# Performance work log

Measured on AMD Instinct MI355X. Metric: run time of the kernel, lower is better.

## Reference

```python
import jax, jax.numpy as jnp
import numpy as np

V, S, D, H = 32000, 1024, 768, 3072
EPS = 1e-5


def pos_encoding(seq_len, dim, dtype=jnp.float32):
    # pe[pos, i] = sin(pos/10000^(i/dim)) if i even else cos(pos/10000^(i/dim))
    pos = jnp.arange(seq_len, dtype=dtype)[:, None]
    i = jnp.arange(dim, dtype=dtype)[None, :]
    ang = pos / jnp.power(jnp.asarray(10000.0, dtype), i / dim)
    even = (jnp.arange(dim) % 2 == 0)[None, :]
    return jnp.where(even, jnp.sin(ang), jnp.cos(ang))


def layernorm2d(x, w, b):
    # normalizes over last two dims (token_size, input_dim), affine params [S, D]
    m = jnp.mean(x, axis=(-2, -1), keepdims=True)
    v = jnp.mean((x - m) ** 2, axis=(-2, -1), keepdims=True)
    return (x - m) / jnp.sqrt(v + EPS) * w + b


def setup_inputs() -> dict:
    key = jax.random.key(0)
    ks = jax.random.split(key, 16)
    sc = 0.02
    emb = jax.random.normal(ks[0], (V, D), jnp.float32) * sc
    emb = emb.at[0].set(0.0)  # padding_idx=0
    inp = {
        "x": jax.random.randint(ks[1], (8, S), 0, V),
        "emb": emb,
        "Wq": jax.random.normal(ks[2], (D, H), jnp.float32) * sc,
        "bq": jnp.zeros((H,), jnp.float32),
        "Wk": jax.random.normal(ks[3], (D, H), jnp.float32) * sc,
        "bk": jnp.zeros((H,), jnp.float32),
        "Wv": jax.random.normal(ks[4], (D, H), jnp.float32) * sc,
        "bv": jnp.zeros((H,), jnp.float32),
        "Wo": jax.random.normal(ks[5], (H, D), jnp.float32) * sc,
        "bo": jnp.zeros((D,), jnp.float32),
        "W1": jax.random.normal(ks[6], (D, H), jnp.float32) * sc,
        "b1": jnp.zeros((H,), jnp.float32),
        "W2": jax.random.normal(ks[7], (H, D), jnp.float32) * sc,
        "b2": jnp.zeros((D,), jnp.float32),
        "ln1_w": jnp.ones((S, D), jnp.float32),
        "ln1_b": jnp.zeros((S, D), jnp.float32),
        "ln2_w": jnp.ones((S, D), jnp.float32),
        "ln2_b": jnp.zeros((S, D), jnp.float32),
    }
    return inp


def reference(x, emb, Wq, bq, Wk, bk, Wv, bv, Wo, bo, W1, b1, W2, b2, ln1_w, ln1_b, ln2_w, ln2_b):
    y = emb[x]                                   # [B, S, D]
    y = y + pos_encoding(y.shape[1], y.shape[2], y.dtype)
    # unscaled self-attention (no 1/sqrt(d) factor, faithful to source)
    q = y @ Wq + bq
    k = y @ Wk + bk
    v = y @ Wv + bv
    attn = jax.nn.softmax(jnp.einsum("bsh,bth->bst", q, k), axis=-1)
    a = jnp.einsum("bst,bth->bsh", attn, v) @ Wo + bo
    y = layernorm2d(y + a, ln1_w, ln1_b)
    # FFN: GELU applied AFTER second linear (faithful to source)
    f = jax.nn.gelu((y @ W1 + b1) @ W2 + b2, approximate=False)
    y = layernorm2d(y + f, ln2_w, ln2_b)
    return y
```

## Files before the change

### kernel.cpp

```cpp
#include <hip/hip_runtime.h>
#include <hip/hip_fp16.h>

#define DI __device__ __forceinline__

typedef _Float16 f16x8 __attribute__((ext_vector_type(8)));
typedef float f32x4 __attribute__((ext_vector_type(4)));

struct alignas(8) h4 { __half x, y, z, w; };

DI void async16(const void* g, void* l) {
  __builtin_amdgcn_global_load_lds(
      (__attribute__((address_space(1))) void*)g,
      (__attribute__((address_space(3))) void*)l, 16, 0, 0);
}

DI float waveReduceSum(float v) {
#pragma unroll
  for (int i = 1; i < 64; i <<= 1) v += __shfl_xor(v, i);
  return v;
}
DI float waveReduceMax(float v) {
#pragma unroll
  for (int i = 1; i < 64; i <<= 1) v = fmaxf(v, __shfl_xor(v, i));
  return v;
}

DI float gelu_exact(float x) { return 0.5f * x * (1.f + erff(x * 0.70710678118654752f)); }

template <typename CT, bool BIAS, bool BROW>
__global__ __launch_bounds__(512, 2) void gemm_nt8(
    const __half* __restrict__ A, int lda, long long sA,
    const __half* __restrict__ Bt, int ldb, long long sB,
    const float* __restrict__ bias, long long sBias,
    CT* __restrict__ C, int ldc, long long sC,
    int nT, int K) {
  __shared__ __align__(16) __half As[2][16384];
  __shared__ __align__(16) __half Bs[2][16384];

  const int tid = threadIdx.x;
  const int wave = tid >> 6, lane = tid & 63;

  const int gsz = 4 * nT;
  const int g = blockIdx.x / gsz, r = blockIdx.x % gsz;
  const int m0 = (g * 4 + (r & 3)) * 256;
  const int n0 = (r >> 2) * 256;

  A += (long long)blockIdx.z * sA;
  Bt += (long long)blockIdx.z * sB;
  C += (long long)blockIdx.z * sC;
  if constexpr (BIAS || BROW) bias += (long long)blockIdx.z * sBias;

  const int wm = wave >> 2, wn = wave & 3;

  f32x4 acc[8][4];
#pragma unroll
  for (int i = 0; i < 8; ++i)
#pragma unroll
    for (int j = 0; j < 4; ++j) acc[i][j] = (f32x4){0.f, 0.f, 0.f, 0.f};

  const int srow = tid >> 3;
  const int gc = (tid & 7) ^ (srow & 7);
  const __half* Ag = A + (size_t)(m0 + srow) * lda + gc * 8;
  const __half* Bg = Bt + (size_t)(n0 + srow) * ldb + gc * 8;
  const size_t a64 = (size_t)64 * lda, b64 = (size_t)64 * ldb;
  char* AsWr = (char*)As + wave * 1024 + lane * 16;
  char* BsWr = (char*)Bs + wave * 1024 + lane * 16;

  f16x8 sra[4], srb[4];

#define LDG(t)                                                        \
  {                                                                   \
    const __half* sa_ = Ag + (t) * 64;                                \
    const __half* sb_ = Bg + (t) * 64;                                \
    sra[0] = *(const f16x8*)(sa_);                                    \
    sra[1] = *(const f16x8*)(sa_ + a64);                              \
    sra[2] = *(const f16x8*)(sa_ + 2 * a64);                          \
    sra[3] = *(const f16x8*)(sa_ + 3 * a64);                          \
    srb[0] = *(const f16x8*)(sb_);                                    \
    srb[1] = *(const f16x8*)(sb_ + b64);                              \
    srb[2] = *(const f16x8*)(sb_ + 2 * b64);                          \
    srb[3] = *(const f16x8*)(sb_ + 3 * b64);                          \
  }
#define DSW(t)                                                        \
  {                                                                   \
    char* da_ = AsWr + (((t) & 1) ? 32768 : 0);                       \
    char* db_ = BsWr + (((t) & 1) ? 32768 : 0);                       \
    *(f16x8*)(da_) = sra[0];                                          \
    *(f16x8*)(da_ + 8192) = sra[1];                                   \
    *(f16x8*)(da_ + 16384) = sra[2];                                  \
    *(f16x8*)(da_ + 24576) = sra[3];                                  \
    *(f16x8*)(db_) = srb[0];                                          \
    *(f16x8*)(db_ + 8192) = srb[1];                                   \
    *(f16x8*)(db_ + 16384) = srb[2];                                  \
    *(f16x8*)(db_ + 24576) = srb[3];                                  \
  }

  const int ml = lane & 15, q = lane >> 4, lx = lane & 7;
  const int co0 = (q ^ lx) * 16, co1 = co0 ^ 64;
  const char* Ar = (const char*)As + wm * 16384 + ml * 128;
  const char* Br = (const char*)Bs + (wn >> 1) * 16384 + (wn & 1) * 8192 + ml * 128;

  const int nt = K >> 6;
  LDG(0);
  DSW(0);
  if (nt > 1) LDG(1);
  asm volatile("s_waitcnt lgkmcnt(0)" ::: "memory");
  __builtin_amdgcn_s_barrier();
  __builtin_amdgcn_sched_barrier(0);

  for (int t = 0; t < nt; ++t) {
    if (t + 1 < nt) {
      DSW(t + 1);
      if (t + 2 < nt) LDG(t + 2);
    }
    const int pb = (t & 1) ? 32768 : 0;
    const char* Ap = Ar + pb;
    const char* Bp = Br + pb;
    f16x8 af[8], bf[4];
#pragma unroll
    for (int ks = 0; ks < 2; ++ks) {
      const int co = ks ? co1 : co0;
#pragma unroll
      for (int i = 0; i < 8; ++i) af[i] = *(const f16x8*)(Ap + i * 2048 + co);
#pragma unroll
      for (int j = 0; j < 4; ++j) bf[j] = *(const f16x8*)(Bp + j * 2048 + co);
#pragma unroll
      for (int i = 0; i < 8; ++i)
#pragma unroll
        for (int j = 0; j < 4; ++j)
          acc[i][j] = __builtin_amdgcn_mfma_f32_16x16x32_f16(bf[j], af[i], acc[i][j], 0, 0, 0);
    }
    asm volatile("s_waitcnt lgkmcnt(0)" ::: "memory");
    __builtin_amdgcn_s_barrier();
    __builtin_amdgcn_sched_barrier(0);
  }
#undef LDG
#undef DSW

#pragma unroll
  for (int j = 0; j < 4; ++j) {
    const int col0 = n0 + wn * 64 + j * 16 + q * 4;
    float4 bc = {0.f, 0.f, 0.f, 0.f};
    if constexpr (BIAS) bc = *(const float4*)(bias + col0);
#pragma unroll
    for (int i = 0; i < 8; ++i) {
      const int row = m0 + wm * 128 + i * 16 + ml;
      const float br = BROW ? bias[row] : 0.f;
      const float v0 = acc[i][j][0] + bc.x + br;
      const float v1 = acc[i][j][1] + bc.y + br;
      const float v2 = acc[i][j][2] + bc.z + br;
      const float v3 = acc[i][j][3] + bc.w + br;
      if constexpr (sizeof(CT) == 4) {
        *(float4*)(C + (size_t)row * ldc + col0) = make_float4(v0, v1, v2, v3);
      } else {
        h4 o{__float2half(v0), __float2half(v1), __float2half(v2), __float2half(v3)};
        *(h4*)((__half*)C + (size_t)row * ldc + col0) = o;
      }
    }
  }
}

template <typename CT, bool BIAS, bool BROW>
__global__ __launch_bounds__(256) void gemm_nt(
    const __half* __restrict__ A, int lda, long long sA,
    const __half* __restrict__ Bt, int ldb, long long sB,
    const float* __restrict__ bias, long long sBias,
    CT* __restrict__ C, int ldc, long long sC,
    int nT, int K) {
  __shared__ __align__(16) __half As[128 * 64];
  __shared__ __align__(16) __half Bs[128 * 64];

  const int tid = threadIdx.x;
  const int wave = tid >> 6, lane = tid & 63;

  const int gsz = 8 * nT;
  const int g = blockIdx.x / gsz, r = blockIdx.x % gsz;
  const int m0 = (g * 8 + (r & 7)) * 128;
  const int n0 = (r >> 3) * 128;

  A += (long long)blockIdx.z * sA;
  Bt += (long long)blockIdx.z * sB;
  C += (long long)blockIdx.z * sC;
  if constexpr (BIAS || BROW) bias += (long long)blockIdx.z * sBias;
  const int wm = wave & 1, wn = wave >> 1;

  f32x4 acc[4][4];
#pragma unroll
  for (int i = 0; i < 4; ++i)
#pragma unroll
    for (int jj = 0; jj < 4; ++jj) acc[i][jj] = (f32x4){0.f, 0.f, 0.f, 0.f};

  const int srow = tid >> 3;
  const int gc = (tid & 7) ^ (srow & 7);
  const __half* Ag = A + (size_t)(m0 + srow) * lda + gc * 8;
  const __half* Bg = Bt + (size_t)(n0 + srow) * ldb + gc * 8;
  const size_t a32 = (size_t)32 * lda, b32 = (size_t)32 * ldb;
  char* AsW = (char*)As + wave * 1024;
  char* BsW = (char*)Bs + wave * 1024;

  const int ml = lane & 15, q = lane >> 4, lx = lane & 7;
  const int aoff = ((wm * 64 + ml) * 8 + (q ^ lx)) * 16;
  const int boff = ((wn * 64 + ml) * 8 + (q ^ lx)) * 16;

  for (int k0 = 0; k0 < K; k0 += 64) {
#pragma unroll
    for (int i = 0; i < 4; ++i) {
      async16(Ag + i * a32 + k0, AsW + i * 4096);
      async16(Bg + i * b32 + k0, BsW + i * 4096);
    }
    __syncthreads();
#pragma unroll
    for (int jj = 0; jj < 2; ++jj) {
      const char* Ab = (const char*)As + (jj ? (aoff ^ 64) : aoff);
      const char* Bb = (const char*)Bs + (jj ? (boff ^ 64) : boff);
      f16x8 af[4], bf[4];
#pragma unroll
      for (int i = 0; i < 4; ++i) {
        af[i] = *(const f16x8*)(Ab + i * 2048);
        bf[i] = *(const f16x8*)(Bb + i * 2048);
      }
#pragma unroll
      for (int i = 0; i < 4; ++i)
#pragma unroll
        for (int jn = 0; jn < 4; ++jn)
          acc[i][jn] = __builtin_amdgcn_mfma_f32_16x16x32_f16(bf[jn], af[i], acc[i][jn], 0, 0, 0);
    }
    __syncthreads();
  }

#pragma unroll
  for (int jn = 0; jn < 4; ++jn) {
    const int col0 = n0 + wn * 64 + jn * 16 + q * 4;
    float4 bc = {0.f, 0.f, 0.f, 0.f};
    if constexpr (BIAS) bc = *(const float4*)(bias + col0);
#pragma unroll
    for (int i = 0; i < 4; ++i) {
      const int row = m0 + wm * 64 + i * 16 + ml;
      const float br = BROW ? bias[row] : 0.f;
      const float v0 = acc[i][jn][0] + bc.x + br;
      const float v1 = acc[i][jn][1] + bc.y + br;
      const float v2 = acc[i][jn][2] + bc.z + br;
      const float v3 = acc[i][jn][3] + bc.w + br;
      if constexpr (sizeof(CT) == 4) {
        *(float4*)(C + (size_t)row * ldc + col0) = make_float4(v0, v1, v2, v3);
      } else {
        h4 o{__float2half(v0), __float2half(v1), __float2half(v2), __float2half(v3)};
        *(h4*)((__half*)C + (size_t)row * ldc + col0) = o;
      }
    }
  }
}

__global__ __launch_bounds__(256) void prep(
    const float* __restrict__ Wq, const float* __restrict__ Wk,
    const float* __restrict__ Wv, const float* __restrict__ W1,
    const float* __restrict__ Wo, const float* __restrict__ W2,
    const float* __restrict__ bq, const float* __restrict__ bk,
    __half* __restrict__ wD, __half* __restrict__ wB, __half* __restrict__ wC,
    __half* __restrict__ wA, float* __restrict__ bqk) {
  if (blockIdx.x == 2304) {
    if (blockIdx.y == 0)
      for (int i = threadIdx.x; i < 3072; i += 256) {
        bqk[i] = bq[i];
        bqk[3072 + i] = bk[i];
      }
    return;
  }
  __shared__ float t[32][33];
  const int tx = threadIdx.x & 31, ty = threadIdx.x >> 5;
  if (blockIdx.y < 4) {
    const float* in;
    __half* out;
    switch (blockIdx.y) {
      case 0: in = Wq; out = wD; break;
      case 1: in = Wk; out = wD + 3072 * 768; break;
      case 2: in = Wv; out = wB; break;
      default: in = W1; out = wC; break;
    }
    const int cb = blockIdx.x % 96, rb = blockIdx.x / 96;
    const int c = cb * 32 + tx, r0 = rb * 32;
#pragma unroll
    for (int i = 0; i < 32; i += 8) t[ty + i][tx] = in[(size_t)(r0 + ty + i) * 3072 + c];
    __syncthreads();
    const int oc = r0 + tx, o0 = cb * 32;
#pragma unroll
    for (int i = 0; i < 32; i += 8)
      out[(size_t)(o0 + ty + i) * 768 + oc] = __float2half(t[tx][ty + i]);
  } else {
    const float* in = (blockIdx.y == 5) ? W2 : Wo;
    __half* out = wA + ((blockIdx.y == 5) ? 3072 * 768 : 0);
    const int cb = blockIdx.x % 24, rb = blockIdx.x / 24;
    const int c = cb * 32 + tx, r0 = rb * 32;
#pragma unroll
    for (int i = 0; i < 32; i += 8) t[ty + i][tx] = in[(size_t)(r0 + ty + i) * 768 + c];
    __syncthreads();
    const int oc = r0 + tx, o0 = cb * 32;
#pragma unroll
    for (int i = 0; i < 32; i += 8)
      out[(size_t)(o0 + ty + i) * 3072 + oc] = __float2half(t[tx][ty + i]);
  }
}

__global__ __launch_bounds__(256) void embed_pos_kernel(
    const int* __restrict__ x, const float* __restrict__ emb,
    float* __restrict__ y, __half* __restrict__ yh) {
  const int row = blockIdx.x;
  const int s = row & 1023;
  const int tok = x[row];
  const float* ep = emb + (size_t)tok * 768;
  float* yp = y + (size_t)row * 768;
  __half* hp = yh + (size_t)row * 768;
  const float c = -13.287712379549449f / 768.f;
  for (int d = threadIdx.x; d < 768; d += 256) {
    float ang = (float)s * exp2f((float)d * c);
    float pe = (d & 1) ? cosf(ang) : sinf(ang);
    float v = ep[d] + pe;
    yp[d] = v;
    hp[d] = __float2half(v);
  }
}

__global__ __launch_bounds__(256) void softmax_rows(
    const float* __restrict__ L, __half* __restrict__ P) {
  const size_t row = blockIdx.x;
  const float4 x = ((const float4*)(L + row * 1024))[threadIdx.x];
  const int wave = threadIdx.x >> 6, lane = threadIdx.x & 63;
  float m = fmaxf(fmaxf(x.x, x.y), fmaxf(x.z, x.w));
  m = waveReduceMax(m);
  __shared__ float sm[4];
  __shared__ float ssum[4];
  if (lane == 0) sm[wave] = m;
  __syncthreads();
  m = fmaxf(fmaxf(sm[0], sm[1]), fmaxf(sm[2], sm[3]));
  float e0 = expf(x.x - m), e1 = expf(x.y - m), e2 = expf(x.z - m), e3 = expf(x.w - m);
  float s = e0 + e1 + e2 + e3;
  s = waveReduceSum(s);
  if (lane == 0) ssum[wave] = s;
  __syncthreads();
  s = ssum[0] + ssum[1] + ssum[2] + ssum[3];
  const float inv = 1.f / s;
  h4 o{__float2half(e0 * inv), __float2half(e1 * inv), __float2half(e2 * inv),
       __float2half(e3 * inv)};
  ((h4*)(P + row * 1024))[threadIdx.x] = o;
}

template <bool GELU>
__global__ __launch_bounds__(256) void residual_stats(
    float* __restrict__ y, const float* __restrict__ p0, const float* __restrict__ p1,
    const float* __restrict__ bias, float2* __restrict__ partials) {
  const int b = blockIdx.y, chunk = blockIdx.x;
  const size_t base = (size_t)b * 786432 + (size_t)chunk * 8192;
  float4* yp = (float4*)(y + base);
  const float4* a0 = (const float4*)(p0 + base);
  const float4* a1 = (const float4*)(p1 + base);
  float s = 0.f, ss = 0.f;
#pragma unroll
  for (int it = 0; it < 8; ++it) {
    const int idx = it * 256 + threadIdx.x;
    const int d = (chunk * 8192 + it * 1024 + threadIdx.x * 4) % 768;
    float4 yv = yp[idx];
    float4 v0 = a0[idx];
    float4 v1 = a1[idx];
    const float4 bv = *(const float4*)(bias + d);
    float ax = v0.x + v1.x + bv.x, ay = v0.y + v1.y + bv.y;
    float az = v0.z + v1.z + bv.z, aw = v0.w + v1.w + bv.w;
    if constexpr (GELU) {
      ax = gelu_exact(ax); ay = gelu_exact(ay);
      az = gelu_exact(az); aw = gelu_exact(aw);
    }
    float4 r{yv.x + ax, yv.y + ay, yv.z + az, yv.w + aw};
    yp[idx] = r;
    s += r.x + r.y + r.z + r.w;
    ss += r.x * r.x + r.y * r.y + r.z * r.z + r.w * r.w;
  }
  s = waveReduceSum(s);
  ss = waveReduceSum(ss);
  __shared__ float2 wr[4];
  const int wave = threadIdx.x >> 6, lane = threadIdx.x & 63;
  if (lane == 0) wr[wave] = make_float2(s, ss);
  __syncthreads();
  if (threadIdx.x == 0) {
    float S = wr[0].x + wr[1].x + wr[2].x + wr[3].x;
    float SS = wr[0].y + wr[1].y + wr[2].y + wr[3].y;
    partials[b * 96 + chunk] = make_float2(S, SS);
  }
}

template <bool WB>
__global__ __launch_bounds__(256) void ln_apply(
    float* __restrict__ y, __half* __restrict__ yh, const float* __restrict__ w,
    const float* __restrict__ bb, const float2* __restrict__ partials) {
  const unsigned i4 = blockIdx.x * 256 + threadIdx.x;
  const unsigned i = i4 * 4;
  const unsigned b = i / 786432u;
  const int tid = threadIdx.x;
  float s = 0.f, ss = 0.f;
  if (tid < 96) {
    float2 p = partials[b * 96 + tid];
    s = p.x;
    ss = p.y;
  }
  s = waveReduceSum(s);
  ss = waveReduceSum(ss);
  __shared__ float2 wsum[4];
  if ((tid & 63) == 0) wsum[tid >> 6] = make_float2(s, ss);
  __syncthreads();
  const float S = wsum[0].x + wsum[1].x + wsum[2].x + wsum[3].x;
  const float SS = wsum[0].y + wsum[1].y + wsum[2].y + wsum[3].y;
  const float inv = 1.f / 786432.f;
  const float mean = S * inv;
  const float rstd = rsqrtf(SS * inv - mean * mean + 1e-5f);

  const unsigned e4 = (i - b * 786432u) >> 2;
  float4 yv = ((const float4*)y)[i4];
  const float4 wv = ((const float4*)w)[e4];
  const float4 bv = ((const float4*)bb)[e4];
  float4 r;
  r.x = (yv.x - mean) * rstd * wv.x + bv.x;
  r.y = (yv.y - mean) * rstd * wv.y + bv.y;
  r.z = (yv.z - mean) * rstd * wv.z + bv.z;
  r.w = (yv.w - mean) * rstd * wv.w + bv.w;
  ((float4*)y)[i4] = r;
  if constexpr (WB) {
    h4 o{__float2half(r.x), __float2half(r.y), __float2half(r.z), __float2half(r.w)};
    ((h4*)yh)[i4] = o;
  }
}

extern "C" void kernel_launch(void* const* d_in, const int* in_sizes, int n_in,
                              void* d_out, int out_size, void* d_ws, size_t ws_size,
                              hipStream_t stream) {
  const int* x = (const int*)d_in[0];
  const float* emb = (const float*)d_in[1];
  const float* Wq = (const float*)d_in[2];
  const float* bq = (const float*)d_in[3];
  const float* Wk = (const float*)d_in[4];
  const float* bk = (const float*)d_in[5];
  const float* Wv = (const float*)d_in[6];
  const float* bv = (const float*)d_in[7];
  const float* Wo = (const float*)d_in[8];
  const float* bo = (const float*)d_in[9];
  const float* W1 = (const float*)d_in[10];
  const float* b1 = (const float*)d_in[11];
  const float* W2 = (const float*)d_in[12];
  const float* b2 = (const float*)d_in[13];
  const float* ln1w = (const float*)d_in[14];
  const float* ln1b = (const float*)d_in[15];
  const float* ln2w = (const float*)d_in[16];
  const float* ln2b = (const float*)d_in[17];

  float* y = (float*)d_out;

  char* ws = (char*)d_ws;
  __half* yh = (__half*)(ws + 0);
  __half* qb = (__half*)(ws + 12582912);
  __half* kb = (__half*)(ws + 62914560);
  __half* Ph = kb;
  __half* vT = (__half*)(ws + 113246208);
  float* abuf = (float*)vT;
  float* Lg = (float*)(ws + 163577856);
  __half* wA = (__half*)(ws + 197132288);
  __half* wD = (__half*)(ws + 206569472);
  __half* wB = (__half*)(ws + 216006656);
  __half* wC = (__half*)(ws + 220725248);
  float* bqk = (float*)(ws + 225443840);
  float2* part = (float2*)(ws + 225468416);
  const size_t WS_NEEDED = 225474624;
  if (ws_size < WS_NEEDED) return;

  const dim3 blk(256), blk8(512);
  const long long SH = 1024LL * 3072, SS = 1024LL * 1024;
  const long long HALF = 25165824;
  float* p1 = abuf + 6291456;

  prep<<<dim3(2305, 6), blk, 0, stream>>>(Wq, Wk, Wv, W1, Wo, W2, bq, bk, wD, wB, wC, wA, bqk);
  embed_pos_kernel<<<dim3(8192), blk, 0, stream>>>(x, emb, y, yh);

  gemm_nt8<__half, true, false><<<dim3(384, 1, 2), blk8, 0, stream>>>(
      yh, 768, 0, wD, 768, 3072LL * 768, bqk, 3072, qb, 3072, HALF, 12, 768);

  gemm_nt<__half, false, true><<<dim3(192, 1, 8), blk, 0, stream>>>(
      wB, 768, 0, yh, 768, 1024LL * 768, bv, 0, vT, 1024, SH, 8, 768);

  gemm_nt<float, false, false><<<dim3(64, 1, 8), blk, 0, stream>>>(
      qb, 3072, SH, kb, 3072, SH, nullptr, 0, Lg, 1024, SS, 8, 3072);

  softmax_rows<<<dim3(8192), blk, 0, stream>>>(Lg, Ph);

  gemm_nt<__half, false, false><<<dim3(192, 1, 8), blk, 0, stream>>>(
      Ph, 1024, SS, vT, 1024, SH, nullptr, 0, (__half*)qb, 3072, SH, 24, 1024);

  gemm_nt<float, false, false><<<dim3(384, 1, 2), blk, 0, stream>>>(
      (__half*)qb, 3072, 1536, wA, 3072, 1536, nullptr, 0, abuf, 768, 6291456, 6, 1536);

  residual_stats<false><<<dim3(96, 8), blk, 0, stream>>>(y, abuf, p1, bo, part);
  ln_apply<true><<<dim3(6144), blk, 0, stream>>>(y, yh, ln1w, ln1b, part);

  gemm_nt<__half, true, false><<<dim3(1536, 1, 1), blk, 0, stream>>>(
      yh, 768, 0, wC, 768, 0, b1, 0, (__half*)qb, 3072, 0, 24, 768);
  gemm_nt<float, false, false><<<dim3(384, 1, 2), blk, 0, stream>>>(
      (__half*)qb, 3072, 1536, wA + 3072 * 768, 3072, 1536, nullptr, 0, abuf, 768, 6291456, 6, 1536);

  residual_stats<true><<<dim3(96, 8), blk, 0, stream>>>(y, abuf, p1, b2, part);
  ln_apply<false><<<dim3(6144), blk, 0, stream>>>(y, nullptr, ln2w, ln2b, part);
}
```

Measured before the change: 743.4 us.

## Rework 256x256 GEMM main loop into a four-phase ping-pong schedule with async LDS loads

The 8-wave 256x256 GEMM drops its register-staged global-to-LDS copies and uses direct global_load_lds async copies, issued in quarters interleaved with MFMA work. Each K-step is split into four MFMA quadrants, separated by barriers and wrapped in s_setprio, so LDS reads, async fills and matrix math overlap. The FFN first linear now launches this 8-wave kernel instead of the 4-wave 128-tile one. The gain would come from fewer VGPRs and better latency hiding. The cost is many more barriers per iteration and tight vmcnt accounting that has to match the number of outstanding loads.

```diff
diff --git a/kernel.cpp b/kernel.cpp
--- a/kernel.cpp
+++ b/kernel.cpp
@@ -26,6 +26,8 @@
 }
 
 DI float gelu_exact(float x) { return 0.5f * x * (1.f + erff(x * 0.70710678118654752f)); }
+
+#define MFMA16(b_, a_, c_) __builtin_amdgcn_mfma_f32_16x16x32_f16((b_), (a_), (c_), 0, 0, 0)
 
 template <typename CT, bool BIAS, bool BROW>
 __global__ __launch_bounds__(512, 2) void gemm_nt8(
@@ -63,36 +65,22 @@
   const __half* Ag = A + (size_t)(m0 + srow) * lda + gc * 8;
   const __half* Bg = Bt + (size_t)(n0 + srow) * ldb + gc * 8;
   const size_t a64 = (size_t)64 * lda, b64 = (size_t)64 * ldb;
-  char* AsWr = (char*)As + wave * 1024 + lane * 16;
-  char* BsWr = (char*)Bs + wave * 1024 + lane * 16;
-
-  f16x8 sra[4], srb[4];
-
-#define LDG(t)                                                        \
-  {                                                                   \
-    const __half* sa_ = Ag + (t) * 64;                                \
-    const __half* sb_ = Bg + (t) * 64;                                \
-    sra[0] = *(const f16x8*)(sa_);                                    \
-    sra[1] = *(const f16x8*)(sa_ + a64);                              \
-    sra[2] = *(const f16x8*)(sa_ + 2 * a64);                          \
-    sra[3] = *(const f16x8*)(sa_ + 3 * a64);                          \
-    srb[0] = *(const f16x8*)(sb_);                                    \
-    srb[1] = *(const f16x8*)(sb_ + b64);                              \
-    srb[2] = *(const f16x8*)(sb_ + 2 * b64);                          \
-    srb[3] = *(const f16x8*)(sb_ + 3 * b64);                          \
-  }
-#define DSW(t)                                                        \
-  {                                                                   \
-    char* da_ = AsWr + (((t) & 1) ? 32768 : 0);                       \
-    char* db_ = BsWr + (((t) & 1) ? 32768 : 0);                       \
-    *(f16x8*)(da_) = sra[0];                                          \
-    *(f16x8*)(da_ + 8192) = sra[1];                                   \
-    *(f16x8*)(da_ + 16384) = sra[2];                                  \
-    *(f16x8*)(da_ + 24576) = sra[3];                                  \
-    *(f16x8*)(db_) = srb[0];                                          \
-    *(f16x8*)(db_ + 8192) = srb[1];                                   \
-    *(f16x8*)(db_ + 16384) = srb[2];                                  \
-    *(f16x8*)(db_ + 24576) = srb[3];                                  \
+  char* AsW = (char*)As + wave * 1024;
+  char* BsW = (char*)Bs + wave * 1024;
+
+#define STG_A(t, h)                                                       \
+  {                                                                       \
+    const __half* s_ = Ag + (size_t)(h) * 128 * lda + (t) * 64;           \
+    char* d_ = AsW + (((t) & 1) ? 32768 : 0) + (h) * 16384;               \
+    async16(s_, d_);                                                      \
+    async16(s_ + a64, d_ + 8192);                                         \
+  }
+#define STG_B(t, h)                                                       \
+  {                                                                       \
+    const __half* s_ = Bg + (size_t)(h) * 128 * ldb + (t) * 64;           \
+    char* d_ = BsW + (((t) & 1) ? 32768 : 0) + (h) * 16384;               \
+    async16(s_, d_);                                                      \
+    async16(s_ + b64, d_ + 8192);                                         \
   }
 
   const int ml = lane & 15, q = lane >> 4, lx = lane & 7;
@@ -101,41 +89,111 @@
   const char* Br = (const char*)Bs + (wn >> 1) * 16384 + (wn & 1) * 8192 + ml * 128;
 
   const int nt = K >> 6;
-  LDG(0);
-  DSW(0);
-  if (nt > 1) LDG(1);
-  asm volatile("s_waitcnt lgkmcnt(0)" ::: "memory");
+  STG_B(0, 0);
+  STG_A(0, 0);
+  STG_A(0, 1);
+  STG_B(0, 1);
+  if (nt > 1) {
+    STG_B(1, 0);
+    asm volatile("s_waitcnt vmcnt(2)" ::: "memory");
+  } else {
+    asm volatile("s_waitcnt vmcnt(0)" ::: "memory");
+  }
   __builtin_amdgcn_s_barrier();
-  __builtin_amdgcn_sched_barrier(0);
+
+  f16x8 al0[4], al1[4], ah0[4], ah1[4];
+  f16x8 bl0[2], bl1[2], bh0[2], bh1[2];
 
   for (int t = 0; t < nt; ++t) {
-    if (t + 1 < nt) {
-      DSW(t + 1);
-      if (t + 2 < nt) LDG(t + 2);
-    }
     const int pb = (t & 1) ? 32768 : 0;
     const char* Ap = Ar + pb;
     const char* Bp = Br + pb;
-    f16x8 af[8], bf[4];
-#pragma unroll
-    for (int ks = 0; ks < 2; ++ks) {
-      const int co = ks ? co1 : co0;
-#pragma unroll
-      for (int i = 0; i < 8; ++i) af[i] = *(const f16x8*)(Ap + i * 2048 + co);
-#pragma unroll
-      for (int j = 0; j < 4; ++j) bf[j] = *(const f16x8*)(Bp + j * 2048 + co);
-#pragma unroll
-      for (int i = 0; i < 8; ++i)
-#pragma unroll
-        for (int j = 0; j < 4; ++j)
-          acc[i][j] = __builtin_amdgcn_mfma_f32_16x16x32_f16(bf[j], af[i], acc[i][j], 0, 0, 0);
-    }
+
+#pragma unroll
+    for (int i = 0; i < 4; ++i) {
+      al0[i] = *(const f16x8*)(Ap + i * 2048 + co0);
+      al1[i] = *(const f16x8*)(Ap + i * 2048 + co1);
+    }
+#pragma unroll
+    for (int j = 0; j < 2; ++j) {
+      bl0[j] = *(const f16x8*)(Bp + j * 2048 + co0);
+      bl1[j] = *(const f16x8*)(Bp + j * 2048 + co1);
+    }
+    if (t + 1 < nt) STG_B(t + 1, 1);
+    __builtin_amdgcn_s_barrier();
     asm volatile("s_waitcnt lgkmcnt(0)" ::: "memory");
-    __builtin_amdgcn_s_barrier();
     __builtin_amdgcn_sched_barrier(0);
-  }
-#undef LDG
-#undef DSW
+    __builtin_amdgcn_s_setprio(1);
+#pragma unroll
+    for (int i = 0; i < 4; ++i)
+#pragma unroll
+      for (int j = 0; j < 2; ++j) acc[i][j] = MFMA16(bl0[j], al0[i], acc[i][j]);
+#pragma unroll
+    for (int i = 0; i < 4; ++i)
+#pragma unroll
+      for (int j = 0; j < 2; ++j) acc[i][j] = MFMA16(bl1[j], al1[i], acc[i][j]);
+    __builtin_amdgcn_s_setprio(0);
+    __builtin_amdgcn_s_barrier();
+
+#pragma unroll
+    for (int i = 0; i < 4; ++i) {
+      ah0[i] = *(const f16x8*)(Ap + (4 + i) * 2048 + co0);
+      ah1[i] = *(const f16x8*)(Ap + (4 + i) * 2048 + co1);
+    }
+    if (t + 1 < nt) STG_A(t + 1, 0);
+    __builtin_amdgcn_s_barrier();
+    asm volatile("s_waitcnt lgkmcnt(0)" ::: "memory");
+    __builtin_amdgcn_sched_barrier(0);
+    __builtin_amdgcn_s_setprio(1);
+#pragma unroll
+    for (int i = 0; i < 4; ++i)
+#pragma unroll
+      for (int j = 0; j < 2; ++j) acc[4 + i][j] = MFMA16(bl0[j], ah0[i], acc[4 + i][j]);
+#pragma unroll
+    for (int i = 0; i < 4; ++i)
+#pragma unroll
+      for (int j = 0; j < 2; ++j) acc[4 + i][j] = MFMA16(bl1[j], ah1[i], acc[4 + i][j]);
+    __builtin_amdgcn_s_setprio(0);
+    __builtin_amdgcn_s_barrier();
+
+#pragma unroll
+    for (int j = 0; j < 2; ++j) {
+      bh0[j] = *(const f16x8*)(Bp + (2 + j) * 2048 + co0);
+      bh1[j] = *(const f16x8*)(Bp + (2 + j) * 2048 + co1);
+    }
+    if (t + 1 < nt) STG_A(t + 1, 1);
+    __builtin_amdgcn_s_barrier();
+    asm volatile("s_waitcnt lgkmcnt(0)" ::: "memory");
+    __builtin_amdgcn_sched_barrier(0);
+    __builtin_amdgcn_s_setprio(1);
+#pragma unroll
+    for (int i = 0; i < 4; ++i)
+#pragma unroll
+      for (int j = 0; j < 2; ++j) acc[4 + i][2 + j] = MFMA16(bh0[j], ah0[i], acc[4 + i][2 + j]);
+#pragma unroll
+    for (int i = 0; i < 4; ++i)
+#pragma unroll
+      for (int j = 0; j < 2; ++j) acc[4 + i][2 + j] = MFMA16(bh1[j], ah1[i], acc[4 + i][2 + j]);
+    __builtin_amdgcn_s_setprio(0);
+    __builtin_amdgcn_s_barrier();
+
+    if (t + 2 < nt) STG_B(t + 2, 0);
+    asm volatile("s_waitcnt vmcnt(2)" ::: "memory");
+    __builtin_amdgcn_s_barrier();
+    __builtin_amdgcn_s_setprio(1);
+#pragma unroll
+    for (int i = 0; i < 4; ++i)
+#pragma unroll
+      for (int j = 0; j < 2; ++j) acc[i][2 + j] = MFMA16(bh0[j], al0[i], acc[i][2 + j]);
+#pragma unroll
+    for (int i = 0; i < 4; ++i)
+#pragma unroll
+      for (int j = 0; j < 2; ++j) acc[i][2 + j] = MFMA16(bh1[j], al1[i], acc[i][2 + j]);
+    __builtin_amdgcn_s_setprio(0);
+    __builtin_amdgcn_s_barrier();
+  }
+#undef STG_A
+#undef STG_B
 
 #pragma unroll
   for (int j = 0; j < 4; ++j) {
@@ -223,7 +281,7 @@
       for (int i = 0; i < 4; ++i)
 #pragma unroll
         for (int jn = 0; jn < 4; ++jn)
-          acc[i][jn] = __builtin_amdgcn_mfma_f32_16x16x32_f16(bf[jn], af[i], acc[i][jn], 0, 0, 0);
+          acc[i][jn] = MFMA16(bf[jn], af[i], acc[i][jn]);
     }
     __syncthreads();
   }
@@ -496,8 +554,8 @@
   residual_stats<false><<<dim3(96, 8), blk, 0, stream>>>(y, abuf, p1, bo, part);
   ln_apply<true><<<dim3(6144), blk, 0, stream>>>(y, yh, ln1w, ln1b, part);
 
-  gemm_nt<__half, true, false><<<dim3(1536, 1, 1), blk, 0, stream>>>(
-      yh, 768, 0, wC, 768, 0, b1, 0, (__half*)qb, 3072, 0, 24, 768);
+  gemm_nt8<__half, true, false><<<dim3(384, 1, 1), blk8, 0, stream>>>(
+      yh, 768, 0, wC, 768, 0, b1, 0, (__half*)qb, 3072, 0, 12, 768);
   gemm_nt<float, false, false><<<dim3(384, 1, 2), blk, 0, stream>>>(
       (__half*)qb, 3072, 1536, wA + 3072 * 768, 3072, 1536, nullptr, 0, abuf, 768, 6291456, 6, 1536);
 
```

After: 746.3 us. About the same (+0.4%).

## Double-buffer gemm_nt with register-staged prefetch instead of synchronous async LDS loads

Applied to the files above, without the earlier changes.

The 128x128 GEMM kernel drops its single-buffer global_load_lds loop, which waited on a barrier before every k-step, and adopts the same register-staged, double-buffered LDS pipeline already used by gemm_nt8. Tile t+2 is loaded from global memory into registers while tile t+1 is written to LDS and tile t is consumed by MFMAs, so memory latency is hidden behind compute. Launch bounds add a minimum of 2 blocks per CU, and LDS use doubles to 64 KB per block. The trade-off is higher register pressure and the loss of the direct-to-LDS load path.

```diff
diff --git a/kernel.cpp b/kernel.cpp
--- a/kernel.cpp
+++ b/kernel.cpp
@@ -8,12 +8,6 @@
 
 struct alignas(8) h4 { __half x, y, z, w; };
 
-DI void async16(const void* g, void* l) {
-  __builtin_amdgcn_global_load_lds(
-      (__attribute__((address_space(1))) void*)g,
-      (__attribute__((address_space(3))) void*)l, 16, 0, 0);
-}
-
 DI float waveReduceSum(float v) {
 #pragma unroll
   for (int i = 1; i < 64; i <<= 1) v += __shfl_xor(v, i);
@@ -26,6 +20,8 @@
 }
 
 DI float gelu_exact(float x) { return 0.5f * x * (1.f + erff(x * 0.70710678118654752f)); }
+
+#define MFMA16(b_, a_, c_) __builtin_amdgcn_mfma_f32_16x16x32_f16((b_), (a_), (c_), 0, 0, 0)
 
 template <typename CT, bool BIAS, bool BROW>
 __global__ __launch_bounds__(512, 2) void gemm_nt8(
@@ -63,8 +59,8 @@
   const __half* Ag = A + (size_t)(m0 + srow) * lda + gc * 8;
   const __half* Bg = Bt + (size_t)(n0 + srow) * ldb + gc * 8;
   const size_t a64 = (size_t)64 * lda, b64 = (size_t)64 * ldb;
-  char* AsWr = (char*)As + wave * 1024 + lane * 16;
-  char* BsWr = (char*)Bs + wave * 1024 + lane * 16;
+  char* AsWr = (char*)As + tid * 16;
+  char* BsWr = (char*)Bs + tid * 16;
 
   f16x8 sra[4], srb[4];
 
@@ -128,7 +124,7 @@
       for (int i = 0; i < 8; ++i)
 #pragma unroll
         for (int j = 0; j < 4; ++j)
-          acc[i][j] = __builtin_amdgcn_mfma_f32_16x16x32_f16(bf[j], af[i], acc[i][j], 0, 0, 0);
+          acc[i][j] = MFMA16(bf[j], af[i], acc[i][j]);
     }
     asm volatile("s_waitcnt lgkmcnt(0)" ::: "memory");
     __builtin_amdgcn_s_barrier();
@@ -161,14 +157,14 @@
 }
 
 template <typename CT, bool BIAS, bool BROW>
-__global__ __launch_bounds__(256) void gemm_nt(
+__global__ __launch_bounds__(256, 2) void gemm_nt(
     const __half* __restrict__ A, int lda, long long sA,
     const __half* __restrict__ Bt, int ldb, long long sB,
     const float* __restrict__ bias, long long sBias,
     CT* __restrict__ C, int ldc, long long sC,
     int nT, int K) {
-  __shared__ __align__(16) __half As[128 * 64];
-  __shared__ __align__(16) __half Bs[128 * 64];
+  __shared__ __align__(16) __half As[2][8192];
+  __shared__ __align__(16) __half Bs[2][8192];
 
   const int tid = threadIdx.x;
   const int wave = tid >> 6, lane = tid & 63;
@@ -195,24 +191,60 @@
   const __half* Ag = A + (size_t)(m0 + srow) * lda + gc * 8;
   const __half* Bg = Bt + (size_t)(n0 + srow) * ldb + gc * 8;
   const size_t a32 = (size_t)32 * lda, b32 = (size_t)32 * ldb;
-  char* AsW = (char*)As + wave * 1024;
-  char* BsW = (char*)Bs + wave * 1024;
+  char* AsWr = (char*)As + tid * 16;
+  char* BsWr = (char*)Bs + tid * 16;
+
+  f16x8 sra[4], srb[4];
+
+#define LDG(t)                                                        \
+  {                                                                   \
+    const __half* sa_ = Ag + (t) * 64;                                \
+    const __half* sb_ = Bg + (t) * 64;                                \
+    sra[0] = *(const f16x8*)(sa_);                                    \
+    sra[1] = *(const f16x8*)(sa_ + a32);                              \
+    sra[2] = *(const f16x8*)(sa_ + 2 * a32);                          \
+    sra[3] = *(const f16x8*)(sa_ + 3 * a32);                          \
+    srb[0] = *(const f16x8*)(sb_);                                    \
+    srb[1] = *(const f16x8*)(sb_ + b32);                              \
+    srb[2] = *(const f16x8*)(sb_ + 2 * b32);                          \
+    srb[3] = *(const f16x8*)(sb_ + 3 * b32);                          \
+  }
+#define DSW(t)                                                        \
+  {                                                                   \
+    char* da_ = AsWr + (((t) & 1) ? 16384 : 0);                       \
+    char* db_ = BsWr + (((t) & 1) ? 16384 : 0);                       \
+    *(f16x8*)(da_) = sra[0];                                          \
+    *(f16x8*)(da_ + 4096) = sra[1];                                   \
+    *(f16x8*)(da_ + 8192) = sra[2];                                   \
+    *(f16x8*)(da_ + 12288) = sra[3];                                  \
+    *(f16x8*)(db_) = srb[0];                                          \
+    *(f16x8*)(db_ + 4096) = srb[1];                                   \
+    *(f16x8*)(db_ + 8192) = srb[2];                                   \
+    *(f16x8*)(db_ + 12288) = srb[3];                                  \
+  }
 
   const int ml = lane & 15, q = lane >> 4, lx = lane & 7;
   const int aoff = ((wm * 64 + ml) * 8 + (q ^ lx)) * 16;
   const int boff = ((wn * 64 + ml) * 8 + (q ^ lx)) * 16;
 
-  for (int k0 = 0; k0 < K; k0 += 64) {
-#pragma unroll
-    for (int i = 0; i < 4; ++i) {
-      async16(Ag + i * a32 + k0, AsW + i * 4096);
-      async16(Bg + i * b32 + k0, BsW + i * 4096);
-    }
-    __syncthreads();
+  const int nt = K >> 6;
+  LDG(0);
+  DSW(0);
+  if (nt > 1) LDG(1);
+  asm volatile("s_waitcnt lgkmcnt(0)" ::: "memory");
+  __builtin_amdgcn_s_barrier();
+  __builtin_amdgcn_sched_barrier(0);
+
+  for (int t = 0; t < nt; ++t) {
+    if (t + 1 < nt) {
+      DSW(t + 1);
+      if (t + 2 < nt) LDG(t + 2);
+    }
+    const int pb = (t & 1) ? 16384 : 0;
 #pragma unroll
     for (int jj = 0; jj < 2; ++jj) {
-      const char* Ab = (const char*)As + (jj ? (aoff ^ 64) : aoff);
-      const char* Bb = (const char*)Bs + (jj ? (boff ^ 64) : boff);
+      const char* Ab = (const char*)As + pb + (jj ? (aoff ^ 64) : aoff);
+      const char* Bb = (const char*)Bs + pb + (jj ? (boff ^ 64) : boff);
       f16x8 af[4], bf[4];
 #pragma unroll
       for (int i = 0; i < 4; ++i) {
@@ -223,10 +255,14 @@
       for (int i = 0; i < 4; ++i)
 #pragma unroll
         for (int jn = 0; jn < 4; ++jn)
-          acc[i][jn] = __builtin_amdgcn_mfma_f32_16x16x32_f16(bf[jn], af[i], acc[i][jn], 0, 0, 0);
-    }
-    __syncthreads();
-  }
+          acc[i][jn] = MFMA16(bf[jn], af[i], acc[i][jn]);
+    }
+    asm volatile("s_waitcnt lgkmcnt(0)" ::: "memory");
+    __builtin_amdgcn_s_barrier();
+    __builtin_amdgcn_sched_barrier(0);
+  }
+#undef LDG
+#undef DSW
 
 #pragma unroll
   for (int jn = 0; jn < 4; ++jn) {
```

Result: no change. 738.5 us (-0.7%).
